# Kernel optimization log

Hardware: AMD Instinct MI355X
Metric: run time of the kernel (lower is better)

## Reference

```python
import jax, jax.numpy as jnp
import numpy as np

TEMPERATURE = 0.1
EPS = 1e-12  # tf.math.l2_normalize epsilon

BATCH = 512
DIM = 256
QUEUE = 65536


def l2_normalize(x, axis=1):
    sq = jnp.sum(x * x, axis=axis, keepdims=True)
    return x * jax.lax.rsqrt(jnp.maximum(sq, EPS))


def setup_inputs() -> dict:
    key = jax.random.key(0)
    k1, k2, k3 = jax.random.split(key, 3)
    projections_1 = jax.random.normal(k1, (BATCH, DIM), dtype=jnp.float32)
    projections_2 = jax.random.normal(k2, (BATCH, DIM), dtype=jnp.float32)
    feature_queue = l2_normalize(jax.random.normal(k3, (QUEUE, DIM), dtype=jnp.float32), axis=1)
    return {"projections_1": projections_1, "projections_2": projections_2, "feature_queue": feature_queue}


def nearest_neighbour(projections, feature_queue):
    # [B, Q] similarity vs the memory queue, 1-NN retrieval + gather
    support_similarities = jnp.einsum('bd,qd->bq', projections, feature_queue)
    nn_idx = jnp.argmax(support_similarities, axis=1)
    nn_projections = feature_queue[nn_idx]  # [B, D]
    # straight-through: forward value is nn, gradient flows to projections
    return projections + jax.lax.stop_gradient(nn_projections - projections)


def reference(projections_1, projections_2, feature_queue):
    p1 = l2_normalize(projections_1, axis=1)
    p2 = l2_normalize(projections_2, axis=1)

    nn1 = nearest_neighbour(p1, feature_queue)
    nn2 = nearest_neighbour(p2, feature_queue)

    s_1_2_1 = jnp.einsum('bd,cd->bc', nn1, p2) / TEMPERATURE
    s_1_2_2 = jnp.einsum('bd,cd->bc', p2, nn1) / TEMPERATURE
    s_2_1_1 = jnp.einsum('bd,cd->bc', nn2, p1) / TEMPERATURE
    s_2_1_2 = jnp.einsum('bd,cd->bc', p1, nn2) / TEMPERATURE

    logits = jnp.concatenate([s_1_2_1, s_1_2_2, s_2_1_1, s_2_1_2], axis=0)  # [4B, B]
    batch = p1.shape[0]
    labels = jnp.tile(jnp.arange(batch), 4)  # [4B]

    # sparse categorical crossentropy from logits
    logp = jax.nn.log_softmax(logits, axis=-1)
    loss = -logp[jnp.arange(4 * batch), labels]  # [4B]

    # FIFO queue update (normalized projections_1 pushed in front)
    new_queue = jnp.concatenate([p1, feature_queue[:-batch]], axis=0)
    return loss, new_queue
```

## Files before the change

### kernel.cpp

```cpp
#include <hip/hip_runtime.h>
#include <stdint.h>


#define BATCH  512
#define DIM    256
#define QUEUE  65536
#define MROWS  1024
#define NGRP   2048
#define MARGIN 0.01f

typedef short bf16x8 __attribute__((ext_vector_type(8)));
typedef float f32x4  __attribute__((ext_vector_type(4)));

__device__ __forceinline__ unsigned int mono_f32(float f) {
    unsigned int u = __float_as_uint(f);
    return (u & 0x80000000u) ? ~u : (u | 0x80000000u);
}
__device__ __forceinline__ float unmono_f32(unsigned int m) {
    unsigned int u = (m & 0x80000000u) ? (m ^ 0x80000000u) : ~m;
    return __uint_as_float(u);
}
__device__ __forceinline__ unsigned short f2bf(float f) {
    unsigned int u = __float_as_uint(f);
    return (unsigned short)((u + 0x7fffu + ((u >> 16) & 1u)) >> 16);
}

__global__ void k1_norm(const float* __restrict__ p1, const float* __restrict__ p2,
                        float* __restrict__ Pn, float* __restrict__ PnT,
                        unsigned short* __restrict__ Phi, float* __restrict__ outq,
                        int* __restrict__ npairs, unsigned int* __restrict__ rowmaxU,
                        unsigned long long* __restrict__ rowfinal)
{
    const int r = blockIdx.x;
    const int t = threadIdx.x;
    if (t == 0) {
        rowmaxU[r] = 0u;
        rowfinal[r] = 0ull;
        if (r == 0) *npairs = 0;
    }
    const float* src = (r < BATCH) ? p1 : p2;
    const int row = (r < BATCH) ? r : r - BATCH;
    float4 v = ((const float4*)(src + (size_t)row * DIM))[t];
    float sq = v.x*v.x + v.y*v.y + v.z*v.z + v.w*v.w;
    #pragma unroll
    for (int off = 32; off; off >>= 1) sq += __shfl_xor(sq, off, 64);
    sq = fmaxf(sq, 1e-12f);
    float s = rsqrtf(sq);
    s = s * (1.5f - 0.5f * sq * s * s);
    v.x *= s; v.y *= s; v.z *= s; v.w *= s;
    ((float4*)(Pn + (size_t)r * DIM))[t] = v;
    const int k = t * 4;
    PnT[(size_t)(k + 0) * MROWS + r] = v.x;
    PnT[(size_t)(k + 1) * MROWS + r] = v.y;
    PnT[(size_t)(k + 2) * MROWS + r] = v.z;
    PnT[(size_t)(k + 3) * MROWS + r] = v.w;
    short4 b;
    b.x = (short)f2bf(v.x); b.y = (short)f2bf(v.y);
    b.z = (short)f2bf(v.z); b.w = (short)f2bf(v.w);
    ((short4*)Phi)[(size_t)r * (DIM / 4) + t] = b;
    if (r < BATCH) ((float4*)(outq + (size_t)r * DIM))[t] = v;
}

__global__ __launch_bounds__(256, 4)
void k2_mfma(const unsigned short* __restrict__ Phi, const float* __restrict__ queue,
             float* __restrict__ outq, float* __restrict__ cand)
{
    __shared__ __align__(16) char Bs[32768];
    const int nt = blockIdx.x;
    const int n0 = nt * 64;
    const int t  = threadIdx.x;
    const int w  = t >> 6, lane = t & 63;
    const int lr = lane & 15, q = lane >> 4;

    {
        const f32x4* qsrc = (const f32x4*)(queue + (size_t)n0 * DIM);
        f32x4* qdst = (f32x4*)(outq + (size_t)(n0 + BATCH) * DIM);
        #pragma unroll 4
        for (int it = 0; it < 16; ++it) {
            const int L = it * 256 + t;
            const int r = L >> 6, h = L & 63;
            f32x4 v = qsrc[(size_t)r * 64 + h];
            if (n0 + r < QUEUE - BATCH)
                __builtin_nontemporal_store(v, qdst + (size_t)r * 64 + h);
            short4 b;
            b.x = (short)f2bf(v.x); b.y = (short)f2bf(v.y);
            b.z = (short)f2bf(v.z); b.w = (short)f2bf(v.w);
            const int c16 = h >> 1, half = h & 1;
            *(short4*)(Bs + r * 512 + ((c16 ^ (r & 31)) << 4) + half * 8) = b;
        }
    }
    __syncthreads();

    const unsigned short* Pw = Phi + (size_t)(w * 64 + lr) * DIM + q * 8;

    for (int mt = 0; mt < 4; ++mt) {
        const int m0 = mt * 256;
        f32x4 acc[4][4];
        #pragma unroll
        for (int i = 0; i < 4; ++i)
            #pragma unroll
            for (int j = 0; j < 4; ++j) acc[i][j] = (f32x4){0.f, 0.f, 0.f, 0.f};

        const unsigned short* Pmt = Pw + (size_t)m0 * DIM;
        #pragma unroll 2
        for (int ks = 0; ks < 8; ++ks) {
            bf16x8 qf[4], pf[4];
            #pragma unroll
            for (int ni = 0; ni < 4; ++ni) {
                const int r = ni * 16 + lr;
                const int c16 = ks * 4 + q;
                qf[ni] = *(const bf16x8*)(Bs + r * 512 + ((c16 ^ (r & 31)) << 4));
            }
            #pragma unroll
            for (int mj = 0; mj < 4; ++mj)
                pf[mj] = *(const bf16x8*)(Pmt + (size_t)mj * 16 * DIM + ks * 32);
            #pragma unroll
            for (int ni = 0; ni < 4; ++ni)
                #pragma unroll
                for (int mj = 0; mj < 4; ++mj)
                    acc[ni][mj] = __builtin_amdgcn_mfma_f32_16x16x32_bf16(qf[ni], pf[mj], acc[ni][mj], 0, 0, 0);
        }

        #pragma unroll
        for (int mj = 0; mj < 4; ++mj) {
            #pragma unroll
            for (int gl = 0; gl < 2; ++gl) {
                f32x4 va = acc[2 * gl][mj], vb = acc[2 * gl + 1][mj];
                float mx = fmaxf(fmaxf(fmaxf(va[0], va[1]), fmaxf(va[2], va[3])),
                                 fmaxf(fmaxf(vb[0], vb[1]), fmaxf(vb[2], vb[3])));
                mx = fmaxf(mx, __shfl_xor(mx, 16, 64));
                mx = fmaxf(mx, __shfl_xor(mx, 32, 64));
                if (q == 0)
                    cand[(size_t)(nt * 2 + gl) * MROWS + (m0 + w * 64 + mj * 16 + lr)] = mx;
            }
        }
    }
}

__global__ void k2b_rowmax(const float* __restrict__ cand, unsigned int* __restrict__ rowmaxU)
{
    const int t  = threadIdx.x;
    const int ml = t & 63, gs = t >> 6;
    const int mc = blockIdx.x & 15, gc = blockIdx.x >> 4;
    const int m  = mc * 64 + ml;
    const int g0 = gc * 128 + gs * 32;
    float mx = -1e30f;
    #pragma unroll 8
    for (int j = 0; j < 32; ++j)
        mx = fmaxf(mx, cand[(size_t)(g0 + j) * MROWS + m]);
    __shared__ float pm[4][64];
    pm[gs][ml] = mx;
    __syncthreads();
    if (gs == 0) {
        mx = fmaxf(fmaxf(pm[0][ml], pm[1][ml]), fmaxf(pm[2][ml], pm[3][ml]));
        atomicMax(rowmaxU + m, mono_f32(mx));
    }
}

__global__ void k2c_filter(const float* __restrict__ cand, const unsigned int* __restrict__ rowmaxU,
                           unsigned int* __restrict__ pairs, int* __restrict__ npairs)
{
    const int t  = threadIdx.x;
    const int ml = t & 63, gs = t >> 6;
    const int mc = blockIdx.x & 15, gc = blockIdx.x >> 4;
    const int m  = mc * 64 + ml;
    const int g0 = gc * 128 + gs * 32;
    const float thr = unmono_f32(rowmaxU[m]) - MARGIN;
    #pragma unroll 8
    for (int j = 0; j < 32; ++j) {
        if (cand[(size_t)(g0 + j) * MROWS + m] >= thr) {
            int p = atomicAdd(npairs, 1);
            pairs[p] = ((unsigned int)m << 16) | (unsigned int)(g0 + j);
        }
    }
}

__global__ __launch_bounds__(256, 4)
void k2d_rescore(const unsigned int* __restrict__ pairs, const int* __restrict__ npairs,
                 const float* __restrict__ Pn, const float* __restrict__ queue,
                 unsigned long long* __restrict__ rowfinal)
{
    const int t = threadIdx.x, w = t >> 6, lane = t & 63;
    const int n = *npairs;
    const int col_l = lane & 31, half = lane >> 5;
    for (int p = blockIdx.x * 4 + w; p < n; p += gridDim.x * 4) {
        const unsigned int pr = pairs[p];
        const int row = pr >> 16, g = pr & 0xffff;
        const int col = g * 32 + col_l;
        const float4* qp = (const float4*)(queue + (size_t)col * DIM + half * 128);
        const float4* pp = (const float4*)(Pn + (size_t)row * DIM + half * 128);
        float4 sv = {0.f, 0.f, 0.f, 0.f};
        #pragma unroll 8
        for (int j = 0; j < 32; ++j) {
            float4 a = pp[j], b = qp[j];
            sv.x = fmaf(a.x, b.x, sv.x); sv.y = fmaf(a.y, b.y, sv.y);
            sv.z = fmaf(a.z, b.z, sv.z); sv.w = fmaf(a.w, b.w, sv.w);
        }
        float s = (sv.x + sv.y) + (sv.z + sv.w);
        s += __shfl_xor(s, 32, 64);
        unsigned long long best = ((unsigned long long)mono_f32(s) << 32)
                                | (unsigned int)(65535 - col);
        #pragma unroll
        for (int off = 1; off <= 16; off <<= 1) {
            unsigned long long o = __shfl_xor(best, off, 64);
            best = best > o ? best : o;
        }
        if (lane == 0) atomicMax(rowfinal + row, best);
    }
}

__global__ void k3_sim(const unsigned long long* __restrict__ rowfinal,
                       const float* __restrict__ queue,
                       const float* __restrict__ PnT, float* __restrict__ S)
{
    const int b  = blockIdx.x;
    const int rb = (b >> 1) * 8;
    const int ch = b & 1;
    const int tid = threadIdx.x;
    const int which = (rb < BATCH) ? 0 : 1;
    const int colbase = which ? 0 : BATCH;
    const int col = colbase + ch * 256 + tid;
    __shared__ float nnv[8][DIM];
    #pragma unroll
    for (int j = 0; j < 8; ++j) {
        const int idx = 65535 - (int)(rowfinal[rb + j] & 0xFFFFull);
        nnv[j][tid] = queue[(size_t)idx * DIM + tid];
    }
    __syncthreads();
    float acc[8];
    #pragma unroll
    for (int j = 0; j < 8; ++j) acc[j] = 0.f;
    for (int k4 = 0; k4 < 64; ++k4) {
        float4 nv[8];
        #pragma unroll
        for (int j = 0; j < 8; ++j) nv[j] = ((const float4*)nnv[j])[k4];
        #pragma unroll
        for (int kk = 0; kk < 4; ++kk) {
            const int k = k4 * 4 + kk;
            const float v0 = PnT[(size_t)k * MROWS + col];
            #pragma unroll
            for (int j = 0; j < 8; ++j) {
                const float nj = ((const float*)&nv[j])[kk];
                acc[j] = fmaf(nj, v0, acc[j]);
            }
        }
    }
    const int i0 = rb & (BATCH - 1);
    float* Sout = S + (size_t)which * (BATCH * BATCH);
    #pragma unroll
    for (int j = 0; j < 8; ++j)
        Sout[(size_t)(i0 + j) * BATCH + ch * 256 + tid] = acc[j] * 10.0f;
}

__global__ void k4_loss(const float* __restrict__ S, float* __restrict__ loss)
{
    const int r = blockIdx.x;
    const int tid = threadIdx.x;
    const int grp = r >> 9;
    const int i = r & 511;
    const float* M = S + (size_t)(grp >> 1) * (BATCH * BATCH);
    float x0, x1;
    if (!(grp & 1)) { x0 = M[(size_t)i * BATCH + tid];  x1 = M[(size_t)i * BATCH + tid + 256]; }
    else            { x0 = M[(size_t)tid * BATCH + i];  x1 = M[(size_t)(tid + 256) * BATCH + i]; }
    const float diag = M[(size_t)i * BATCH + i];
    float mx = fmaxf(x0, x1);
    #pragma unroll
    for (int off = 1; off < 64; off <<= 1) mx = fmaxf(mx, __shfl_xor(mx, off, 64));
    __shared__ float redm[4], reds[4];
    if ((tid & 63) == 0) redm[tid >> 6] = mx;
    __syncthreads();
    mx = fmaxf(fmaxf(redm[0], redm[1]), fmaxf(redm[2], redm[3]));
    float e = __expf(x0 - mx) + __expf(x1 - mx);
    #pragma unroll
    for (int off = 1; off < 64; off <<= 1) e += __shfl_xor(e, off, 64);
    if ((tid & 63) == 0) reds[tid >> 6] = e;
    __syncthreads();
    if (tid == 0)
        loss[r] = mx + logf(reds[0] + reds[1] + reds[2] + reds[3]) - diag;
}

extern "C" void kernel_launch(void* const* d_in, const int* in_sizes, int n_in,
                              void* d_out, int out_size, void* d_ws, size_t ws_size,
                              hipStream_t stream)
{
    const float* p1    = (const float*)d_in[0];
    const float* p2    = (const float*)d_in[1];
    const float* queue = (const float*)d_in[2];
    float* out  = (float*)d_out;
    float* loss = out;
    float* outq = out + 4 * BATCH;

    char* w = (char*)d_ws;
    float* cand = (float*)w;                               w += (size_t)NGRP * MROWS * 4;
    unsigned long long* rowfinal = (unsigned long long*)w; w += MROWS * 8;
    unsigned int* rowmaxU = (unsigned int*)w;              w += MROWS * 4;
    float* Pn  = (float*)w;                                w += (size_t)MROWS * DIM * 4;
    float* PnT = (float*)w;                                w += (size_t)MROWS * DIM * 4;
    unsigned short* Phi = (unsigned short*)w;              w += (size_t)MROWS * DIM * 2;
    float* S = (float*)w;                                  w += (size_t)2 * BATCH * BATCH * 4;
    unsigned int* pairs = (unsigned int*)w;                w += (size_t)NGRP * MROWS * 4;
    int* npairs = (int*)w;

    hipLaunchKernelGGL(k1_norm,     dim3(MROWS), dim3(64),  0, stream, p1, p2, Pn, PnT, Phi, outq,
                       npairs, rowmaxU, rowfinal);
    hipLaunchKernelGGL(k2_mfma,     dim3(QUEUE / 64), dim3(256), 0, stream, Phi, queue, outq, cand);
    hipLaunchKernelGGL(k2b_rowmax,  dim3(256),   dim3(256), 0, stream, cand, rowmaxU);
    hipLaunchKernelGGL(k2c_filter,  dim3(256),   dim3(256), 0, stream, cand, rowmaxU, pairs, npairs);
    hipLaunchKernelGGL(k2d_rescore, dim3(512),   dim3(256), 0, stream, pairs, npairs, Pn, queue, rowfinal);
    hipLaunchKernelGGL(k3_sim,      dim3(256),   dim3(256), 0, stream, rowfinal, queue, PnT, S);
    hipLaunchKernelGGL(k4_loss,     dim3(4 * BATCH), dim3(256), 0, stream, S, loss);
}
```

Measured before the change: 258.6 us.

## Keep projection fragments in registers and double-buffer queue tiles across M-slices

The k2 similarity kernel changes decomposition. Previously each block staged one 64-row queue tile and looped over all 1024 projection rows. Now each block owns one 256-row M-slice, keeps its projection bf16 fragments resident in registers, and streams four 64-row queue tiles through double-buffered LDS. This removes repeated global reloads of the projection operand, but each queue tile is now read and converted four times (once per M-slice), with only slice 0 writing the queue copy. It also raises register pressure and halves the occupancy target, and the stage-next-tile step is not truly asynchronous, since loads happen after the epilogue before the barrier.

```diff
diff --git a/kernel.cpp b/kernel.cpp
--- a/kernel.cpp
+++ b/kernel.cpp
@@ -61,64 +61,77 @@
     if (r < BATCH) ((float4*)(outq + (size_t)r * DIM))[t] = v;
 }
 
-__global__ __launch_bounds__(256, 4)
+__device__ __forceinline__ void k2_stage(const float* __restrict__ queue,
+                                         float* __restrict__ outq,
+                                         char* Bsb, int nr, int tid, bool docopy)
+{
+    const f32x4* qsrc = (const f32x4*)(queue + (size_t)nr * DIM);
+    f32x4* qdst = (f32x4*)(outq + (size_t)(nr + BATCH) * DIM);
+    #pragma unroll 4
+    for (int it = 0; it < 16; ++it) {
+        const int L = it * 256 + tid;
+        const int r = L >> 6, h = L & 63;
+        f32x4 v = qsrc[(size_t)r * 64 + h];
+        if (docopy && (nr + r < QUEUE - BATCH))
+            __builtin_nontemporal_store(v, qdst + (size_t)r * 64 + h);
+        short4 b;
+        b.x = (short)f2bf(v.x); b.y = (short)f2bf(v.y);
+        b.z = (short)f2bf(v.z); b.w = (short)f2bf(v.w);
+        const int c16 = h >> 1, hf = h & 1;
+        *(short4*)(Bsb + r * 512 + ((c16 ^ (r & 31)) << 4) + hf * 8) = b;
+    }
+}
+
+__global__ __launch_bounds__(256, 2)
 void k2_mfma(const unsigned short* __restrict__ Phi, const float* __restrict__ queue,
              float* __restrict__ outq, float* __restrict__ cand)
 {
-    __shared__ __align__(16) char Bs[32768];
-    const int nt = blockIdx.x;
-    const int n0 = nt * 64;
+    __shared__ __align__(16) char Bs[2][32768];
+    const int bid = blockIdx.x;
+    const int s = bid >> 8;
+    const int c = bid & 255;
     const int t  = threadIdx.x;
     const int w  = t >> 6, lane = t & 63;
     const int lr = lane & 15, q = lane >> 4;
-
+    const int mbase = s * 256 + w * 64;
+    const int n0 = c * 256;
+    const bool docopy = (s == 0);
+
+    bf16x8 pfr[4][8];
     {
-        const f32x4* qsrc = (const f32x4*)(queue + (size_t)n0 * DIM);
-        f32x4* qdst = (f32x4*)(outq + (size_t)(n0 + BATCH) * DIM);
-        #pragma unroll 4
-        for (int it = 0; it < 16; ++it) {
-            const int L = it * 256 + t;
-            const int r = L >> 6, h = L & 63;
-            f32x4 v = qsrc[(size_t)r * 64 + h];
-            if (n0 + r < QUEUE - BATCH)
-                __builtin_nontemporal_store(v, qdst + (size_t)r * 64 + h);
-            short4 b;
-            b.x = (short)f2bf(v.x); b.y = (short)f2bf(v.y);
-            b.z = (short)f2bf(v.z); b.w = (short)f2bf(v.w);
-            const int c16 = h >> 1, half = h & 1;
-            *(short4*)(Bs + r * 512 + ((c16 ^ (r & 31)) << 4) + half * 8) = b;
-        }
-    }
-    __syncthreads();
-
-    const unsigned short* Pw = Phi + (size_t)(w * 64 + lr) * DIM + q * 8;
-
-    for (int mt = 0; mt < 4; ++mt) {
-        const int m0 = mt * 256;
+        const unsigned short* Pw = Phi + (size_t)(mbase + lr) * DIM + q * 8;
+        #pragma unroll
+        for (int mj = 0; mj < 4; ++mj)
+            #pragma unroll
+            for (int ks = 0; ks < 8; ++ks)
+                pfr[mj][ks] = *(const bf16x8*)(Pw + (size_t)mj * 16 * DIM + ks * 32);
+    }
+
+    k2_stage(queue, outq, Bs[0], n0, t, docopy);
+    __syncthreads();
+
+    for (int tl = 0; tl < 4; ++tl) {
+        char* Bsb = Bs[tl & 1];
         f32x4 acc[4][4];
         #pragma unroll
         for (int i = 0; i < 4; ++i)
             #pragma unroll
             for (int j = 0; j < 4; ++j) acc[i][j] = (f32x4){0.f, 0.f, 0.f, 0.f};
 
-        const unsigned short* Pmt = Pw + (size_t)m0 * DIM;
-        #pragma unroll 2
+        #pragma unroll
         for (int ks = 0; ks < 8; ++ks) {
-            bf16x8 qf[4], pf[4];
+            bf16x8 qf[4];
             #pragma unroll
             for (int ni = 0; ni < 4; ++ni) {
                 const int r = ni * 16 + lr;
                 const int c16 = ks * 4 + q;
-                qf[ni] = *(const bf16x8*)(Bs + r * 512 + ((c16 ^ (r & 31)) << 4));
+                qf[ni] = *(const bf16x8*)(Bsb + r * 512 + ((c16 ^ (r & 31)) << 4));
             }
-            #pragma unroll
-            for (int mj = 0; mj < 4; ++mj)
-                pf[mj] = *(const bf16x8*)(Pmt + (size_t)mj * 16 * DIM + ks * 32);
             #pragma unroll
             for (int ni = 0; ni < 4; ++ni)
                 #pragma unroll
                 for (int mj = 0; mj < 4; ++mj)
-                    acc[ni][mj] = __builtin_amdgcn_mfma_f32_16x16x32_bf16(qf[ni], pf[mj], acc[ni][mj], 0, 0, 0);
+                    acc[ni][mj] = __builtin_amdgcn_mfma_f32_16x16x32_bf16(qf[ni], pfr[mj][ks], acc[ni][mj], 0, 0, 0);
         }
 
         #pragma unroll
@@ -131,9 +144,13 @@
                 mx = fmaxf(mx, __shfl_xor(mx, 16, 64));
                 mx = fmaxf(mx, __shfl_xor(mx, 32, 64));
                 if (q == 0)
-                    cand[(size_t)(nt * 2 + gl) * MROWS + (m0 + w * 64 + mj * 16 + lr)] = mx;
+                    cand[(size_t)(c * 8 + tl * 2 + gl) * MROWS + (mbase + mj * 16 + lr)] = mx;
             }
         }
+
+        if (tl < 3)
+            k2_stage(queue, outq, Bs[(tl + 1) & 1], n0 + (tl + 1) * 64, t, docopy);
+        __syncthreads();
     }
 }
 
@@ -303,7 +320,7 @@
 
     hipLaunchKernelGGL(k1_norm,     dim3(MROWS), dim3(64),  0, stream, p1, p2, Pn, PnT, Phi, outq,
                        npairs, rowmaxU, rowfinal);
-    hipLaunchKernelGGL(k2_mfma,     dim3(QUEUE / 64), dim3(256), 0, stream, Phi, queue, outq, cand);
+    hipLaunchKernelGGL(k2_mfma,     dim3(1024), dim3(256), 0, stream, Phi, queue, outq, cand);
     hipLaunchKernelGGL(k2b_rowmax,  dim3(256),   dim3(256), 0, stream, cand, rowmaxU);
     hipLaunchKernelGGL(k2c_filter,  dim3(256),   dim3(256), 0, stream, cand, rowmaxU, pairs, npairs);
     hipLaunchKernelGGL(k2d_rescore, dim3(512),   dim3(256), 0, stream, pairs, npairs, Pn, queue, rowfinal);
```

New measurement: 265.8 us. 1.03x slower.
